# Kernel tuning notes

Hardware: AMD Instinct MI355X
Metric: run time of the kernel (lower is better)

The kernel has to match this reference:

```python
import jax, jax.numpy as jnp
import numpy as np

B1, B2, R, L, D, H = 48, 48, 36, 30, 1024, 4
EPS = 1e-8


def _l2norm(x):
    return x / (jnp.sqrt(jnp.sum(x * x, axis=-1, keepdims=True)) + EPS)


def _summary_attn(x, w1, b1, w2, b2):
    # x: (B1,B2,N,D). MLP scores -> softmax over N -> weighted mean over H heads.
    h = jax.nn.relu(jnp.einsum('abnd,ed->abne', x, w1) + b1)
    s = jnp.einsum('abne,he->abnh', h, w2) + b2          # (B1,B2,N,H)
    p = jax.nn.softmax(jnp.swapaxes(s, -1, -2), axis=-1)  # (B1,B2,H,N)
    w = jnp.einsum('abhn,abnd->abhd', p, x)               # (B1,B2,H,D)
    return w.mean(axis=-2)                                # (B1,B2,D)


def setup_inputs() -> dict:
    key = jax.random.key(0)
    ks = jax.random.split(key, 12)
    r = np.sqrt(6.0) / np.sqrt(D + D)  # xavier uniform as in init_weights
    return {
        'v1': jax.random.normal(ks[0], (B1, R, D), dtype=jnp.float32),
        'v2': jax.random.normal(ks[1], (B2, L, D), dtype=jnp.float32),
        'w_img': jax.random.uniform(ks[2], (D, D), jnp.float32, -r, r),
        'w_txt': jax.random.uniform(ks[3], (D, D), jnp.float32, -r, r),
        'w1a': jax.random.normal(ks[4], (D, D), jnp.float32) * 0.02,
        'b1a': jnp.zeros((D,), jnp.float32),
        'w2a': jax.random.normal(ks[5], (H, D), jnp.float32) * 0.02,
        'b2a': jnp.zeros((H,), jnp.float32),
        'w1b': jax.random.normal(ks[6], (D, D), jnp.float32) * 0.02,
        'b1b': jnp.zeros((D,), jnp.float32),
        'w2b': jax.random.normal(ks[7], (H, D), jnp.float32) * 0.02,
        'b2b': jnp.zeros((H,), jnp.float32),
    }


def reference(v1, v2, w_img, w_txt, w1a, b1a, w2a, b2a, w1b, b1b, w2b, b2b):
    d = v1.shape[-1]
    inv_sqrt_d = np.float32(1.0 / np.sqrt(d))
    k1 = jnp.einsum('ard,ed->are', v1, w_img)  # (B1,R,D)
    k2 = jnp.einsum('bld,ed->ble', v2, w_txt)  # (B2,L,D)

    # qkv_attention(k2, k1, v1): queries=words, keys/values=regions
    s1 = jnp.einsum('bld,ard->ablr', k2, k1) * inv_sqrt_d   # (B1,B2,L,R)
    p1 = jax.nn.softmax(s1, axis=-1)
    fused_v2 = jnp.einsum('ablr,ard->abld', p1, v1)         # weighted_v1 -> fused_v2

    # qkv_attention(k1, k2, v2): queries=regions, keys/values=words
    s2 = jnp.einsum('ard,bld->abrl', k1, k2) * inv_sqrt_d   # (B1,B2,R,L)
    p2 = jax.nn.softmax(s2, axis=-1)
    fused_v1 = jnp.einsum('abrl,bld->abrd', p2, v2)         # weighted_v2 -> fused_v1

    co_v1 = _l2norm(_summary_attn(fused_v1, w1a, b1a, w2a, b2a))
    co_v2 = _l2norm(_summary_attn(fused_v2, w1b, b1b, w2b, b2b))
    return jnp.sum(co_v1 * co_v2, axis=-1)  # (B1,B2) score matrix
```

## Files before the change

kernel.cpp:

```cpp
#include <hip/hip_runtime.h>

#define D 1024
#define NB1 48
#define NB2 48
#define RR 36
#define LL 30
#define NH 4

typedef short bf16x8 __attribute__((ext_vector_type(8)));
typedef float f32x4 __attribute__((ext_vector_type(4)));
typedef float f32x2 __attribute__((ext_vector_type(2)));
typedef unsigned short u16x8 __attribute__((ext_vector_type(8)));

#define MFMA16(a, b, c) __builtin_amdgcn_mfma_f32_16x16x32_bf16(a, b, c, 0, 0, 0)

__device__ __forceinline__ unsigned short f2bf(float x) {
  unsigned u = __float_as_uint(x);
  u += 0x7FFF + ((u >> 16) & 1);
  return (unsigned short)(u >> 16);
}
__device__ __forceinline__ float bf2f(unsigned short h) {
  return __uint_as_float(((unsigned)h) << 16);
}
__device__ __forceinline__ void split8(const float* v, bf16x8& h8, bf16x8& l8) {
  u16x8 hi, lo;
#pragma unroll
  for (int i = 0; i < 8; ++i) {
    unsigned short h = f2bf(v[i]);
    hi[i] = h;
    lo[i] = f2bf(v[i] - bf2f(h));
  }
  h8 = __builtin_bit_cast(bf16x8, hi);
  l8 = __builtin_bit_cast(bf16x8, lo);
}
__device__ __forceinline__ f32x2 shflx2(f32x2 v, int m) {
  double d = __builtin_bit_cast(double, v);
  d = __shfl_xor(d, m);
  return __builtin_bit_cast(f32x2, d);
}

__device__ __forceinline__ void conv_body(const float* __restrict__ X,
                                          unsigned short* __restrict__ out,
                                          int rows, int g) {
  const int lane = threadIdx.x & 63;
  const int tile = g >> 5, kc = g & 31;
  const int row = tile * 16 + (lane & 15);
  const int k = kc * 32 + (lane >> 4) * 8;
  float v[8];
  if (row < rows) {
    const float4* s = (const float4*)(X + (size_t)row * 1024 + k);
    float4 x0 = s[0], x1 = s[1];
    v[0] = x0.x; v[1] = x0.y; v[2] = x0.z; v[3] = x0.w;
    v[4] = x1.x; v[5] = x1.y; v[6] = x1.z; v[7] = x1.w;
  } else {
#pragma unroll
    for (int i = 0; i < 8; ++i) v[i] = 0.f;
  }
  bf16x8 hi, lo;
  split8(v, hi, lo);
  bf16x8* o = (bf16x8*)(out + (size_t)g * 1024 + lane * 8);
  o[0] = hi;
  o[64] = lo;
}

__global__ __launch_bounds__(256) void conv6(
    const float* __restrict__ v1, const float* __restrict__ v2,
    const float* __restrict__ wimg, const float* __restrict__ wtxt,
    const float* __restrict__ w1a, const float* __restrict__ w1b,
    unsigned short* v1f, unsigned short* v2f, unsigned short* wimgf,
    unsigned short* wtxtf, unsigned short* w1af, unsigned short* w1bf) {
  const float* X; unsigned short* O; int rows;
  switch (blockIdx.y) {
    case 0: X = v1; O = v1f; rows = 1728; break;
    case 1: X = v2; O = v2f; rows = 1440; break;
    case 2: X = wimg; O = wimgf; rows = 1024; break;
    case 3: X = wtxt; O = wtxtf; rows = 1024; break;
    case 4: X = w1a; O = w1af; rows = 1024; break;
    default: X = w1b; O = w1bf; rows = 1024; break;
  }
  const int tiles = (rows + 15) >> 4;
  const int g = blockIdx.x * 4 + (threadIdx.x >> 6);
  if (g >= tiles * 32) return;
  conv_body(X, O, rows, g);
}

__global__ __launch_bounds__(256) void conv_k(const float* __restrict__ k1,
                                              const float* __restrict__ k2,
                                              unsigned short* k1f, unsigned short* k2f) {
  const float* X = blockIdx.y ? k2 : k1;
  unsigned short* O = blockIdx.y ? k2f : k1f;
  const int rows = blockIdx.y ? 1440 : 1728;
  const int tiles = (rows + 15) >> 4;
  const int g = blockIdx.x * 4 + (threadIdx.x >> 6);
  if (g >= tiles * 32) return;
  conv_body(X, O, rows, g);
}

__global__ __launch_bounds__(256) void convG(const float* __restrict__ G2a,
                                             const float* __restrict__ G1b,
                                             const float* __restrict__ w2a,
                                             const float* __restrict__ w2b,
                                             unsigned short* G2aF, unsigned short* G1bF,
                                             float4* __restrict__ w2at,
                                             float4* __restrict__ w2bt) {
  const int t = threadIdx.x, lane = t & 63;
  if (blockIdx.y == 0 && blockIdx.x < 4) {
    int col = blockIdx.x * 256 + t;
    w2at[col] = make_float4(w2a[col], w2a[1024 + col], w2a[2048 + col], w2a[3072 + col]);
    w2bt[col] = make_float4(w2b[col], w2b[1024 + col], w2b[2048 + col], w2b[3072 + col]);
  }
  const int bb = blockIdx.x >> 4;
  const int nt = ((blockIdx.x & 15) << 2) + (t >> 6);
  const int c = lane & 15, q = lane >> 4;
  if (blockIdx.y == 0) {
    float v[8];
#pragma unroll
    for (int j = 0; j < 8; ++j) {
      int l = q * 8 + j;
      v[j] = (l < LL) ? G2a[(size_t)(bb * LL + l) * D + nt * 16 + c] : 0.f;
    }
    bf16x8 hi, lo;
    split8(v, hi, lo);
    bf16x8* o = (bf16x8*)(G2aF + ((size_t)(bb * 64 + nt) * 2) * 512 + lane * 8);
    o[0] = hi;
    o[64] = lo;
  } else {
#pragma unroll
    for (int kc = 0; kc < 2; ++kc) {
      float v[8];
#pragma unroll
      for (int j = 0; j < 8; ++j) {
        int r = kc * 32 + q * 8 + j;
        v[j] = (r < RR) ? G1b[(size_t)(bb * RR + r) * D + nt * 16 + c] : 0.f;
      }
      bf16x8 hi, lo;
      split8(v, hi, lo);
      bf16x8* o = (bf16x8*)(G1bF + (((size_t)(bb * 64 + nt) * 2 + kc) * 2) * 512 + lane * 8);
      o[0] = hi;
      o[64] = lo;
    }
  }
}

#define LOAD_FRAGS(AH, AL, BH, BL)                                              \
  {                                                                             \
    _Pragma("unroll") for (int i = 0; i < 4; ++i) {                             \
      AH[i] = Af[ab[i]]; AL[i] = Af[ab[i] + 64]; ab[i] += 128;                  \
    }                                                                           \
    _Pragma("unroll") for (int j = 0; j < 4; ++j) {                             \
      BH[j] = Bf[bb[j]]; BL[j] = Bf[bb[j] + 64]; bb[j] += 128;                  \
    }                                                                           \
  }

#define MFMA_SET(AH, AL, BH, BL)                                                \
  _Pragma("unroll") for (int i = 0; i < 4; ++i)                                 \
      _Pragma("unroll") for (int j = 0; j < 4; ++j) {                           \
    acc[i][j] = MFMA16(AH[i], BH[j], acc[i][j]);                                \
    acc[i][j] = MFMA16(AL[i], BH[j], acc[i][j]);                                \
    acc[i][j] = MFMA16(AH[i], BL[j], acc[i][j]);                                \
  }

__device__ __forceinline__ void gemm4_body(const bf16x8* __restrict__ Af,
                                           const bf16x8* __restrict__ Bf,
                                           float* __restrict__ C,
                                           int M, int N, float scale,
                                           int Mtiles, int Ntiles) {
  const int lane = threadIdx.x & 63;
  const int w = threadIdx.x >> 6;
  const int mb = blockIdx.y * 8 + (w >> 1) * 4;
  const int nb = blockIdx.x * 8 + (w & 1) * 4;
  int ab[4], bb[4];
#pragma unroll
  for (int i = 0; i < 4; ++i) {
    int tm = mb + i; if (tm > Mtiles - 1) tm = Mtiles - 1;
    ab[i] = tm * 4096 + lane;
    int tn = nb + i; if (tn > Ntiles - 1) tn = Ntiles - 1;
    bb[i] = tn * 4096 + lane;
  }
  f32x4 acc[4][4];
#pragma unroll
  for (int i = 0; i < 4; ++i)
#pragma unroll
    for (int j = 0; j < 4; ++j) acc[i][j] = (f32x4){0.f, 0.f, 0.f, 0.f};

  bf16x8 ahA[4], alA[4], bhA[4], blA[4];
  bf16x8 ahB[4], alB[4], bhB[4], blB[4];
  LOAD_FRAGS(ahA, alA, bhA, blA);
#pragma unroll 1
  for (int kc = 0; kc < 30; kc += 2) {
    LOAD_FRAGS(ahB, alB, bhB, blB);
    MFMA_SET(ahA, alA, bhA, blA);
    LOAD_FRAGS(ahA, alA, bhA, blA);
    MFMA_SET(ahB, alB, bhB, blB);
  }
  LOAD_FRAGS(ahB, alB, bhB, blB);
  MFMA_SET(ahA, alA, bhA, blA);
  MFMA_SET(ahB, alB, bhB, blB);

  const int c16 = lane & 15, q = lane >> 4;
#pragma unroll
  for (int i = 0; i < 4; ++i) {
#pragma unroll
    for (int reg = 0; reg < 4; ++reg) {
      int r = (mb + i) * 16 + q * 4 + reg;
      if (r < M) {
#pragma unroll
        for (int j = 0; j < 4; ++j) {
          int col = (nb + j) * 16 + c16;
          if (col < N) C[(size_t)r * N + col] = acc[i][j][reg] * scale;
        }
      }
    }
  }
}

__global__ __launch_bounds__(256) void proj_fused(
    const bf16x8* __restrict__ v1f, const bf16x8* __restrict__ v2f,
    const bf16x8* __restrict__ wimgf, const bf16x8* __restrict__ wtxtf,
    const bf16x8* __restrict__ w1af, const bf16x8* __restrict__ w1bf,
    float* k1, float* k2, float* G2a, float* G1b) {
  const int z = blockIdx.z;
  const bf16x8* Af = (z == 0 || z == 3) ? v1f : v2f;
  const bf16x8* Bf = (z == 0) ? wimgf : (z == 1) ? wtxtf : (z == 2) ? w1af : w1bf;
  float* C = (z == 0) ? k1 : (z == 1) ? k2 : (z == 2) ? G2a : G1b;
  const int M = (z == 0 || z == 3) ? 1728 : 1440;
  const int Mt = (z == 0 || z == 3) ? 108 : 92;
  if ((int)blockIdx.y * 8 >= Mt) return;
  gemm4_body(Af, Bf, C, M, 1024, 1.f, Mt, 64);
}

__global__ __launch_bounds__(256) void cross_s(
    const bf16x8* __restrict__ k2f, const bf16x8* __restrict__ k1f,
    float* Sbuf) {
  gemm4_body(k2f, k1f, Sbuf, 1440, 1728, 0.03125f, 92, 108);
}

__global__ __launch_bounds__(128) void pair_dir(
    const float* __restrict__ Sb,
    const float* __restrict__ v1, const float* __restrict__ v2,
    const bf16x8* __restrict__ G2aF, const bf16x8* __restrict__ G1bF,
    const float* __restrict__ b1a, const float4* __restrict__ w2at, const float* __restrict__ b2a,
    const float* __restrict__ b1b, const float4* __restrict__ w2bt, const float* __restrict__ b2b,
    float* __restrict__ YA, float* __restrict__ YB,
    float* __restrict__ N1buf, float* __restrict__ N2buf) {
  const int pair = blockIdx.x;
  const int a = pair / NB2;
  const int b = pair - a * NB2;
  const int t = threadIdx.x, lane = t & 63, w = t >> 6;
  const int c16 = lane & 15, q = lane >> 4;

  union SM {
    struct {
      float p2s[48][36];
      float red[2][48][4];
      float sa[RR][NH];
      float qa[RR];
      float u2[LL];
      float rb[2];
    } A;
    struct {
      float p1s[32][68];
      float red[2][48][4];
      float sbm[LL][NH];
      float qb[LL];
      float u1[RR];
      float rb[2];
    } B;
  };
  __shared__ __align__(16) SM sm;

  const float* Sab = Sb + (size_t)b * LL * 1728 + (size_t)a * RR;

  if (blockIdx.y == 0) {
    for (int i = t; i < 48 * 36; i += 128) {
      int r = i / 36, c = i - r * 36;
      if (r >= RR || c >= LL) ((float*)sm.A.p2s)[i] = 0.f;
    }
    for (int i = t; i < LL * RR; i += 128) {
      int l = i / RR, r = i - l * RR;
      sm.A.p2s[r][l] = Sab[(size_t)l * 1728 + r];
    }
    __syncthreads();
    if (t < RR * 2) {
      int r = t >> 1, half = t & 1;
      float m = -1e30f;
      for (int l = half; l < LL; l += 2) m = fmaxf(m, sm.A.p2s[r][l]);
      m = fmaxf(m, __shfl_xor(m, 1));
      float s = 0.f;
      for (int l = half; l < LL; l += 2) {
        float e = __expf(sm.A.p2s[r][l] - m);
        sm.A.p2s[r][l] = e;
        s += e;
      }
      s += __shfl_xor(s, 1);
      float inv = 1.f / s;
      for (int l = half; l < LL; l += 2) sm.A.p2s[r][l] *= inv;
    }
    __syncthreads();

    bf16x8 pAh[3], pAl[3];
#pragma unroll
    for (int mt = 0; mt < 3; ++mt) {
      float v[8];
      const float* rp = &sm.A.p2s[mt * 16 + c16][q * 8];
      float4 x0 = *(const float4*)rp;
      float4 x1 = *(const float4*)(rp + 4);
      v[0] = x0.x; v[1] = x0.y; v[2] = x0.z; v[3] = x0.w;
      v[4] = x1.x; v[5] = x1.y; v[6] = x1.z; v[7] = x1.w;
      split8(v, pAh[mt], pAl[mt]);
    }

    f32x2 sc01[3][4], sc23[3][4];
#pragma unroll
    for (int mt = 0; mt < 3; ++mt)
#pragma unroll
      for (int reg = 0; reg < 4; ++reg) {
        sc01[mt][reg] = (f32x2){0.f, 0.f};
        sc23[mt][reg] = (f32x2){0.f, 0.f};
      }

    const bf16x8* gA = G2aF + ((size_t)(b * 64 + w) * 2) * 64 + lane;
#pragma unroll 2
    for (int it = 0; it < 32; ++it) {
      const bf16x8* gp = gA + (size_t)it * 256;
      bf16x8 Bh = gp[0], Bl = gp[64];
      const int col = (w + it * 2) * 16 + c16;
      float4 wv = w2at[col];
      float bias = b1a[col];
      f32x2 w01 = {wv.x, wv.y}, w23 = {wv.z, wv.w};
#pragma unroll
      for (int mt = 0; mt < 3; ++mt) {
        f32x4 acc = {bias, bias, bias, bias};
        acc = MFMA16(pAh[mt], Bh, acc);
        acc = MFMA16(pAl[mt], Bh, acc);
        acc = MFMA16(pAh[mt], Bl, acc);
#pragma unroll
        for (int reg = 0; reg < 4; ++reg) {
          float hv = fmaxf(acc[reg], 0.f);
          f32x2 hv2 = {hv, hv};
          sc01[mt][reg] += hv2 * w01;
          sc23[mt][reg] += hv2 * w23;
        }
      }
    }
#pragma unroll
    for (int mt = 0; mt < 3; ++mt)
#pragma unroll
      for (int reg = 0; reg < 4; ++reg) {
        f32x2 v01 = sc01[mt][reg], v23 = sc23[mt][reg];
#pragma unroll
        for (int m = 1; m <= 8; m <<= 1) {
          v01 += shflx2(v01, m);
          v23 += shflx2(v23, m);
        }
        if (c16 == 0) {
          f32x2* rp = (f32x2*)&sm.A.red[w][mt * 16 + q * 4 + reg][0];
          rp[0] = v01;
          rp[1] = v23;
        }
      }
    __syncthreads();
    for (int i = t; i < RR * NH; i += 128) {
      int r = i >> 2, h = i & 3;
      sm.A.sa[r][h] = sm.A.red[0][r][h] + sm.A.red[1][r][h] + b2a[h];
    }
    __syncthreads();
    if (t < 64) {
      const int h = t >> 4, i = t & 15;
      float x0 = sm.A.sa[i][h];
      float x1 = sm.A.sa[i + 16][h];
      float x2 = (i < 4) ? sm.A.sa[i + 32][h] : -1e30f;
      float m = fmaxf(fmaxf(x0, x1), x2);
      m = fmaxf(m, __shfl_xor(m, 1));
      m = fmaxf(m, __shfl_xor(m, 2));
      m = fmaxf(m, __shfl_xor(m, 4));
      m = fmaxf(m, __shfl_xor(m, 8));
      float e0 = __expf(x0 - m), e1 = __expf(x1 - m);
      float e2 = (i < 4) ? __expf(x2 - m) : 0.f;
      float s = e0 + e1 + e2;
      s += __shfl_xor(s, 1);
      s += __shfl_xor(s, 2);
      s += __shfl_xor(s, 4);
      s += __shfl_xor(s, 8);
      float inv = 1.f / s;
      sm.A.sa[i][h] = e0 * inv;
      sm.A.sa[i + 16][h] = e1 * inv;
      if (i < 4) sm.A.sa[i + 32][h] = e2 * inv;
    }
    __syncthreads();
    if (t < RR)
      sm.A.qa[t] = 0.25f * (sm.A.sa[t][0] + sm.A.sa[t][1] + sm.A.sa[t][2] + sm.A.sa[t][3]);
    __syncthreads();
    if (t < LL * 2) {
      int l = t >> 1, half = t & 1;
      float x = 0.f;
      for (int r = half; r < RR; r += 2) x = fmaf(sm.A.qa[r], sm.A.p2s[r][l], x);
      x += __shfl_xor(x, 1);
      if (half == 0) sm.A.u2[l] = x;
    }
    __syncthreads();
    {
      const float* V2b = v2 + ((size_t)b * LL) * D + t * 8;
      float4 y0 = {0.f, 0.f, 0.f, 0.f}, y1 = {0.f, 0.f, 0.f, 0.f};
      for (int l = 0; l < LL; ++l) {
        float ul = sm.A.u2[l];
        float4 aa = *(const float4*)(V2b + (size_t)l * D);
        float4 cc = *(const float4*)(V2b + (size_t)l * D + 4);
        y0.x = fmaf(ul, aa.x, y0.x); y0.y = fmaf(ul, aa.y, y0.y);
        y0.z = fmaf(ul, aa.z, y0.z); y0.w = fmaf(ul, aa.w, y0.w);
        y1.x = fmaf(ul, cc.x, y1.x); y1.y = fmaf(ul, cc.y, y1.y);
        y1.z = fmaf(ul, cc.z, y1.z); y1.w = fmaf(ul, cc.w, y1.w);
      }
      float4* Yo = (float4*)(YA + (size_t)pair * 1024 + t * 8);
      Yo[0] = y0;
      Yo[1] = y1;
      float pn1 = y0.x * y0.x + y0.y * y0.y + y0.z * y0.z + y0.w * y0.w +
                  y1.x * y1.x + y1.y * y1.y + y1.z * y1.z + y1.w * y1.w;
#pragma unroll
      for (int off = 32; off; off >>= 1) pn1 += __shfl_down(pn1, off);
      if (lane == 0) sm.A.rb[w] = pn1;
      __syncthreads();
      if (t == 0) N1buf[pair] = sm.A.rb[0] + sm.A.rb[1];
    }
  } else {
    for (int i = t; i < 32 * 68; i += 128) {
      int l = i / 68, c = i - l * 68;
      if (l >= LL || c >= RR) ((float*)sm.B.p1s)[i] = 0.f;
    }
    for (int i = t; i < LL * RR; i += 128) {
      int l = i / RR, r = i - l * RR;
      sm.B.p1s[l][r] = Sab[(size_t)l * 1728 + r];
    }
    __syncthreads();
    if (t < LL * 2) {
      int l = t >> 1, half = t & 1;
      float m = -1e30f;
      for (int r = half; r < RR; r += 2) m = fmaxf(m, sm.B.p1s[l][r]);
      m = fmaxf(m, __shfl_xor(m, 1));
      float s = 0.f;
      for (int r = half; r < RR; r += 2) {
        float e = __expf(sm.B.p1s[l][r] - m);
        sm.B.p1s[l][r] = e;
        s += e;
      }
      s += __shfl_xor(s, 1);
      float inv = 1.f / s;
      for (int r = half; r < RR; r += 2) sm.B.p1s[l][r] *= inv;
    }
    __syncthreads();

    bf16x8 pBh[2][2], pBl[2][2];
#pragma unroll
    for (int mt = 0; mt < 2; ++mt)
#pragma unroll
      for (int kc = 0; kc < 2; ++kc) {
        float v[8];
        const float* rp = &sm.B.p1s[mt * 16 + c16][kc * 32 + q * 8];
        float4 x0 = *(const float4*)rp;
        float4 x1 = *(const float4*)(rp + 4);
        v[0] = x0.x; v[1] = x0.y; v[2] = x0.z; v[3] = x0.w;
        v[4] = x1.x; v[5] = x1.y; v[6] = x1.z; v[7] = x1.w;
        split8(v, pBh[mt][kc], pBl[mt][kc]);
      }

    f32x2 sc01[2][4], sc23[2][4];
#pragma unroll
    for (int mt = 0; mt < 2; ++mt)
#pragma unroll
      for (int reg = 0; reg < 4; ++reg) {
        sc01[mt][reg] = (f32x2){0.f, 0.f};
        sc23[mt][reg] = (f32x2){0.f, 0.f};
      }

    const bf16x8* gB = G1bF + ((size_t)(a * 64 + w) * 4) * 64 + lane;
#pragma unroll 2
    for (int it = 0; it < 32; ++it) {
      const bf16x8* gp = gB + (size_t)it * 512;
      bf16x8 B0h = gp[0], B0l = gp[64], B1h = gp[128], B1l = gp[192];
      const int col = (w + it * 2) * 16 + c16;
      float4 wv = w2bt[col];
      float bias = b1b[col];
      f32x2 w01 = {wv.x, wv.y}, w23 = {wv.z, wv.w};
#pragma unroll
      for (int mt = 0; mt < 2; ++mt) {
        f32x4 acc = {bias, bias, bias, bias};
        acc = MFMA16(pBh[mt][0], B0h, acc);
        acc = MFMA16(pBl[mt][0], B0h, acc);
        acc = MFMA16(pBh[mt][0], B0l, acc);
        acc = MFMA16(pBh[mt][1], B1h, acc);
        acc = MFMA16(pBl[mt][1], B1h, acc);
        acc = MFMA16(pBh[mt][1], B1l, acc);
#pragma unroll
        for (int reg = 0; reg < 4; ++reg) {
          float hv = fmaxf(acc[reg], 0.f);
          f32x2 hv2 = {hv, hv};
          sc01[mt][reg] += hv2 * w01;
          sc23[mt][reg] += hv2 * w23;
        }
      }
    }
#pragma unroll
    for (int mt = 0; mt < 2; ++mt)
#pragma unroll
      for (int reg = 0; reg < 4; ++reg) {
        f32x2 v01 = sc01[mt][reg], v23 = sc23[mt][reg];
#pragma unroll
        for (int m = 1; m <= 8; m <<= 1) {
          v01 += shflx2(v01, m);
          v23 += shflx2(v23, m);
        }
        if (c16 == 0) {
          f32x2* rp = (f32x2*)&sm.B.red[w][mt * 16 + q * 4 + reg][0];
          rp[0] = v01;
          rp[1] = v23;
        }
      }
    __syncthreads();
    for (int i = t; i < LL * NH; i += 128) {
      int l = i >> 2, h = i & 3;
      sm.B.sbm[l][h] = sm.B.red[0][l][h] + sm.B.red[1][l][h] + b2b[h];
    }
    __syncthreads();
    if (t < 64) {
      const int h = t >> 4, i = t & 15;
      float x0 = sm.B.sbm[i][h];
      float x1 = (i < 14) ? sm.B.sbm[i + 16][h] : -1e30f;
      float m = fmaxf(x0, x1);
      m = fmaxf(m, __shfl_xor(m, 1));
      m = fmaxf(m, __shfl_xor(m, 2));
      m = fmaxf(m, __shfl_xor(m, 4));
      m = fmaxf(m, __shfl_xor(m, 8));
      float e0 = __expf(x0 - m);
      float e1 = (i < 14) ? __expf(x1 - m) : 0.f;
      float s = e0 + e1;
      s += __shfl_xor(s, 1);
      s += __shfl_xor(s, 2);
      s += __shfl_xor(s, 4);
      s += __shfl_xor(s, 8);
      float inv = 1.f / s;
      sm.B.sbm[i][h] = e0 * inv;
      if (i < 14) sm.B.sbm[i + 16][h] = e1 * inv;
    }
    __syncthreads();
    if (t < LL)
      sm.B.qb[t] = 0.25f * (sm.B.sbm[t][0] + sm.B.sbm[t][1] + sm.B.sbm[t][2] + sm.B.sbm[t][3]);
    __syncthreads();
    if (t < RR * 2) {
      int r = t >> 1, half = t & 1;
      float x = 0.f;
      for (int l = half; l < LL; l += 2) x = fmaf(sm.B.qb[l], sm.B.p1s[l][r], x);
      x += __shfl_xor(x, 1);
      if (half == 0) sm.B.u1[r] = x;
    }
    __syncthreads();
    {
      const float* V1a = v1 + ((size_t)a * RR) * D + t * 8;
      float4 y0 = {0.f, 0.f, 0.f, 0.f}, y1 = {0.f, 0.f, 0.f, 0.f};
      for (int r = 0; r < RR; ++r) {
        float ur = sm.B.u1[r];
        float4 aa = *(const float4*)(V1a + (size_t)r * D);
        float4 cc = *(const float4*)(V1a + (size_t)r * D + 4);
        y0.x = fmaf(ur, aa.x, y0.x); y0.y = fmaf(ur, aa.y, y0.y);
        y0.z = fmaf(ur, aa.z, y0.z); y0.w = fmaf(ur, aa.w, y0.w);
        y1.x = fmaf(ur, cc.x, y1.x); y1.y = fmaf(ur, cc.y, y1.y);
        y1.z = fmaf(ur, cc.z, y1.z); y1.w = fmaf(ur, cc.w, y1.w);
      }
      float4* Yo = (float4*)(YB + (size_t)pair * 1024 + t * 8);
      Yo[0] = y0;
      Yo[1] = y1;
      float pn2 = y0.x * y0.x + y0.y * y0.y + y0.z * y0.z + y0.w * y0.w +
                  y1.x * y1.x + y1.y * y1.y + y1.z * y1.z + y1.w * y1.w;
#pragma unroll
      for (int off = 32; off; off >>= 1) pn2 += __shfl_down(pn2, off);
      if (lane == 0) sm.B.rb[w] = pn2;
      __syncthreads();
      if (t == 0) N2buf[pair] = sm.B.rb[0] + sm.B.rb[1];
    }
  }
}

__global__ __launch_bounds__(128) void pair_final(
    const float* __restrict__ YA, const float* __restrict__ YB,
    const float* __restrict__ N1buf, const float* __restrict__ N2buf,
    float* __restrict__ out) {
  const int pair = blockIdx.x;
  const int t = threadIdx.x;
  const float4* ya = (const float4*)(YA + (size_t)pair * 1024);
  const float4* yb = (const float4*)(YB + (size_t)pair * 1024);
  float s = 0.f;
#pragma unroll
  for (int i = 0; i < 2; ++i) {
    float4 a = ya[t + i * 128], b = yb[t + i * 128];
    s += a.x * b.x + a.y * b.y + a.z * b.z + a.w * b.w;
  }
#pragma unroll
  for (int off = 32; off; off >>= 1) s += __shfl_down(s, off);
  __shared__ float r2[2];
  if ((t & 63) == 0) r2[t >> 6] = s;
  __syncthreads();
  if (t == 0) {
    float num = r2[0] + r2[1];
    float n1 = sqrtf(fmaxf(N1buf[pair], 0.f));
    float n2 = sqrtf(fmaxf(N2buf[pair], 0.f));
    out[pair] = num / ((n1 + 1e-8f) * (n2 + 1e-8f));
  }
}

extern "C" void kernel_launch(void* const* d_in, const int* in_sizes, int n_in,
                              void* d_out, int out_size, void* d_ws, size_t ws_size,
                              hipStream_t stream) {
  const float* v1    = (const float*)d_in[0];
  const float* v2    = (const float*)d_in[1];
  const float* w_img = (const float*)d_in[2];
  const float* w_txt = (const float*)d_in[3];
  const float* w1a   = (const float*)d_in[4];
  const float* b1a   = (const float*)d_in[5];
  const float* w2a   = (const float*)d_in[6];
  const float* b2a   = (const float*)d_in[7];
  const float* w1b   = (const float*)d_in[8];
  const float* b1b   = (const float*)d_in[9];
  const float* w2b   = (const float*)d_in[10];
  const float* b2b   = (const float*)d_in[11];
  float* out = (float*)d_out;

  float* ws   = (float*)d_ws;
  float* k1   = ws;
  float* k2   = k1 + (size_t)1728 * 1024;
  float* G2a  = k2 + (size_t)1440 * 1024;
  float* G1b  = G2a + (size_t)1440 * 1024;
  float* Sbuf = G1b + (size_t)1728 * 1024;
  float* Cbuf = Sbuf + (size_t)1440 * 1728;
  float* g22  = Cbuf + (size_t)1440 * 1728;
  float* g11  = g22 + (size_t)48 * 900;
  (void)g22; (void)g11;

  unsigned short* fb    = (unsigned short*)(g11 + (size_t)48 * 1296);
  unsigned short* v1f   = fb;
  unsigned short* v2f   = v1f + (size_t)108 * 32768;
  unsigned short* k1f   = v2f + (size_t)92 * 32768;
  unsigned short* k2f   = k1f + (size_t)108 * 32768;
  unsigned short* wimgf = k2f + (size_t)92 * 32768;
  unsigned short* wtxtf = wimgf + (size_t)64 * 32768;
  unsigned short* w1af  = wtxtf + (size_t)64 * 32768;
  unsigned short* w1bf  = w1af + (size_t)64 * 32768;
  unsigned short* G2aF  = w1bf + (size_t)64 * 32768;
  unsigned short* G1bF  = G2aF + (size_t)48 * 65536;

  float4* w2at = (float4*)k1;
  float4* w2bt = w2at + 1024;

  float* YA = Cbuf;
  float* YB = (float*)k1f;
  float* N1buf = G2a;
  float* N2buf = N1buf + 2304;

  conv6<<<dim3(864, 6), 256, 0, stream>>>(v1, v2, w_img, w_txt, w1a, w1b,
                                          v1f, v2f, wimgf, wtxtf, w1af, w1bf);

  proj_fused<<<dim3(8, 14, 4), 256, 0, stream>>>(
      (const bf16x8*)v1f, (const bf16x8*)v2f, (const bf16x8*)wimgf,
      (const bf16x8*)wtxtf, (const bf16x8*)w1af, (const bf16x8*)w1bf,
      k1, k2, G2a, G1b);

  conv_k<<<dim3(864, 2), 256, 0, stream>>>(k1, k2, k1f, k2f);
  convG<<<dim3(768, 2), 256, 0, stream>>>(G2a, G1b, w2a, w2b, G2aF, G1bF, w2at, w2bt);

  cross_s<<<dim3(14, 12), 256, 0, stream>>>(
      (const bf16x8*)k2f, (const bf16x8*)k1f, Sbuf);

  pair_dir<<<dim3(2304, 2), 128, 0, stream>>>(
      Sbuf, v1, v2, (const bf16x8*)G2aF, (const bf16x8*)G1bF,
      b1a, w2at, b2a, b1b, w2bt, b2b, YA, YB, N1buf, N2buf);
  pair_final<<<2304, 128, 0, stream>>>(YA, YB, N1buf, N2buf, out);
}
```

Measured before the change: 313.2 us.

## Give each wavefront one pair-direction and batch the value projection per block

pair_dir now gives each 64-lane wave a whole (pair, direction) task. Per-wave shared memory and sched barriers replace the block-wide __syncthreads, and each wave loops over all 64 column tiles itself. The final weighted sum over v1/v2 moves into a new y_batch kernel that reuses each loaded v row across all 48 partners held in registers. pair_final now computes the norms itself. The aim is to cut sync overhead and repeated global reads of v. In exchange it adds a kernel launch, MFMA setprio hints and more register pressure from the 48-entry accumulators.

```diff
diff --git a/kernel.cpp b/kernel.cpp
--- a/kernel.cpp
+++ b/kernel.cpp
@@ -235,74 +235,56 @@
   gemm4_body(k2f, k1f, Sbuf, 1440, 1728, 0.03125f, 92, 108);
 }
 
-__global__ __launch_bounds__(128) void pair_dir(
+__global__ __launch_bounds__(256, 4) void pair_dir(
     const float* __restrict__ Sb,
-    const float* __restrict__ v1, const float* __restrict__ v2,
     const bf16x8* __restrict__ G2aF, const bf16x8* __restrict__ G1bF,
     const float* __restrict__ b1a, const float4* __restrict__ w2at, const float* __restrict__ b2a,
     const float* __restrict__ b1b, const float4* __restrict__ w2bt, const float* __restrict__ b2b,
-    float* __restrict__ YA, float* __restrict__ YB,
-    float* __restrict__ N1buf, float* __restrict__ N2buf) {
-  const int pair = blockIdx.x;
+    float* __restrict__ U1buf, float* __restrict__ U2buf) {
+  const int t = threadIdx.x, lane = t & 63, w = t >> 6;
+  const int id = blockIdx.x * 4 + w;
+  const int pair = id >> 1, dir = id & 1;
   const int a = pair / NB2;
   const int b = pair - a * NB2;
-  const int t = threadIdx.x, lane = t & 63, w = t >> 6;
   const int c16 = lane & 15, q = lane >> 4;
 
-  union SM {
-    struct {
-      float p2s[48][36];
-      float red[2][48][4];
-      float sa[RR][NH];
-      float qa[RR];
-      float u2[LL];
-      float rb[2];
-    } A;
-    struct {
-      float p1s[32][68];
-      float red[2][48][4];
-      float sbm[LL][NH];
-      float qb[LL];
-      float u1[RR];
-      float rb[2];
-    } B;
+  union WSM {
+    struct { float p2s[48][36]; float sa[48][NH]; float qa[48]; } A;
+    struct { float p1s[32][68]; float sbm[32][NH]; float qb[32]; } B;
   };
-  __shared__ __align__(16) SM sm;
-
-  const float* Sab = Sb + (size_t)b * LL * 1728 + (size_t)a * RR;
-
-  if (blockIdx.y == 0) {
-    for (int i = t; i < 48 * 36; i += 128) {
-      int r = i / 36, c = i - r * 36;
-      if (r >= RR || c >= LL) ((float*)sm.A.p2s)[i] = 0.f;
-    }
-    for (int i = t; i < LL * RR; i += 128) {
+  __shared__ __align__(16) WSM sm[4];
+  WSM& S = sm[w];
+
+  const float* Sab = Sb + (size_t)(b * LL) * 1728 + a * RR;
+
+  if (dir == 0) {
+    for (int i = lane; i < 48 * 36; i += 64) ((float*)S.A.p2s)[i] = 0.f;
+    __builtin_amdgcn_sched_barrier(0);
+    for (int i = lane; i < LL * RR; i += 64) {
       int l = i / RR, r = i - l * RR;
-      sm.A.p2s[r][l] = Sab[(size_t)l * 1728 + r];
-    }
-    __syncthreads();
-    if (t < RR * 2) {
-      int r = t >> 1, half = t & 1;
+      S.A.p2s[r][l] = Sab[(size_t)l * 1728 + r];
+    }
+    __builtin_amdgcn_sched_barrier(0);
+    if (lane < RR) {
+      const int r = lane;
       float m = -1e30f;
-      for (int l = half; l < LL; l += 2) m = fmaxf(m, sm.A.p2s[r][l]);
-      m = fmaxf(m, __shfl_xor(m, 1));
+      for (int l = 0; l < LL; ++l) m = fmaxf(m, S.A.p2s[r][l]);
       float s = 0.f;
-      for (int l = half; l < LL; l += 2) {
-        float e = __expf(sm.A.p2s[r][l] - m);
-        sm.A.p2s[r][l] = e;
+      for (int l = 0; l < LL; ++l) {
+        float e = __expf(S.A.p2s[r][l] - m);
+        S.A.p2s[r][l] = e;
         s += e;
       }
-      s += __shfl_xor(s, 1);
       float inv = 1.f / s;
-      for (int l = half; l < LL; l += 2) sm.A.p2s[r][l] *= inv;
-    }
-    __syncthreads();
+      for (int l = 0; l < LL; ++l) S.A.p2s[r][l] *= inv;
+    }
+    __builtin_amdgcn_sched_barrier(0);
 
     bf16x8 pAh[3], pAl[3];
 #pragma unroll
     for (int mt = 0; mt < 3; ++mt) {
       float v[8];
-      const float* rp = &sm.A.p2s[mt * 16 + c16][q * 8];
+      const float* rp = &S.A.p2s[mt * 16 + c16][q * 8];
       float4 x0 = *(const float4*)rp;
       float4 x1 = *(const float4*)(rp + 4);
       v[0] = x0.x; v[1] = x0.y; v[2] = x0.z; v[3] = x0.w;
@@ -319,21 +301,23 @@
         sc23[mt][reg] = (f32x2){0.f, 0.f};
       }
 
-    const bf16x8* gA = G2aF + ((size_t)(b * 64 + w) * 2) * 64 + lane;
+    const bf16x8* gA = G2aF + (size_t)(b * 64) * 128 + lane;
 #pragma unroll 2
-    for (int it = 0; it < 32; ++it) {
-      const bf16x8* gp = gA + (size_t)it * 256;
+    for (int it = 0; it < 64; ++it) {
+      const bf16x8* gp = gA + (size_t)it * 128;
       bf16x8 Bh = gp[0], Bl = gp[64];
-      const int col = (w + it * 2) * 16 + c16;
+      const int col = it * 16 + c16;
       float4 wv = w2at[col];
       float bias = b1a[col];
       f32x2 w01 = {wv.x, wv.y}, w23 = {wv.z, wv.w};
 #pragma unroll
       for (int mt = 0; mt < 3; ++mt) {
         f32x4 acc = {bias, bias, bias, bias};
+        __builtin_amdgcn_s_setprio(1);
         acc = MFMA16(pAh[mt], Bh, acc);
         acc = MFMA16(pAl[mt], Bh, acc);
         acc = MFMA16(pAh[mt], Bl, acc);
+        __builtin_amdgcn_s_setprio(0);
 #pragma unroll
         for (int reg = 0; reg < 4; ++reg) {
           float hv = fmaxf(acc[reg], 0.f);
@@ -343,6 +327,7 @@
         }
       }
     }
+    f32x2 b01 = {b2a[0], b2a[1]}, b23 = {b2a[2], b2a[3]};
 #pragma unroll
     for (int mt = 0; mt < 3; ++mt)
 #pragma unroll
@@ -354,22 +339,17 @@
           v23 += shflx2(v23, m);
         }
         if (c16 == 0) {
-          f32x2* rp = (f32x2*)&sm.A.red[w][mt * 16 + q * 4 + reg][0];
-          rp[0] = v01;
-          rp[1] = v23;
+          f32x2* rp = (f32x2*)&S.A.sa[mt * 16 + q * 4 + reg][0];
+          rp[0] = v01 + b01;
+          rp[1] = v23 + b23;
         }
       }
-    __syncthreads();
-    for (int i = t; i < RR * NH; i += 128) {
-      int r = i >> 2, h = i & 3;
-      sm.A.sa[r][h] = sm.A.red[0][r][h] + sm.A.red[1][r][h] + b2a[h];
-    }
-    __syncthreads();
-    if (t < 64) {
-      const int h = t >> 4, i = t & 15;
-      float x0 = sm.A.sa[i][h];
-      float x1 = sm.A.sa[i + 16][h];
-      float x2 = (i < 4) ? sm.A.sa[i + 32][h] : -1e30f;
+    __builtin_amdgcn_sched_barrier(0);
+    {
+      const int h = q, i = c16;
+      float x0 = S.A.sa[i][h];
+      float x1 = S.A.sa[i + 16][h];
+      float x2 = (i < 4) ? S.A.sa[i + 32][h] : -1e30f;
       float m = fmaxf(fmaxf(x0, x1), x2);
       m = fmaxf(m, __shfl_xor(m, 1));
       m = fmaxf(m, __shfl_xor(m, 2));
@@ -382,72 +362,46 @@
       s += __shfl_xor(s, 2);
       s += __shfl_xor(s, 4);
       s += __shfl_xor(s, 8);
+      float inv = 0.25f / s;
+      float p0 = e0 * inv, p1 = e1 * inv, p2v = e2 * inv;
+      p0 += __shfl_xor(p0, 16); p0 += __shfl_xor(p0, 32);
+      p1 += __shfl_xor(p1, 16); p1 += __shfl_xor(p1, 32);
+      p2v += __shfl_xor(p2v, 16); p2v += __shfl_xor(p2v, 32);
+      if (q == 0) {
+        S.A.qa[i] = p0;
+        S.A.qa[i + 16] = p1;
+        if (i < 4) S.A.qa[i + 32] = p2v;
+      }
+    }
+    __builtin_amdgcn_sched_barrier(0);
+    if (lane < LL) {
+      const int l = lane;
+      float x = 0.f;
+      for (int r = 0; r < RR; ++r) x = fmaf(S.A.qa[r], S.A.p2s[r][l], x);
+      U2buf[((size_t)b * 48 + a) * 32 + l] = x;
+    }
+  } else {
+    for (int i = lane; i < 32 * 68; i += 64) ((float*)S.B.p1s)[i] = 0.f;
+    __builtin_amdgcn_sched_barrier(0);
+    for (int i = lane; i < LL * RR; i += 64) {
+      int l = i / RR, r = i - l * RR;
+      S.B.p1s[l][r] = Sab[(size_t)l * 1728 + r];
+    }
+    __builtin_amdgcn_sched_barrier(0);
+    if (lane < LL) {
+      const int l = lane;
+      float m = -1e30f;
+      for (int r = 0; r < RR; ++r) m = fmaxf(m, S.B.p1s[l][r]);
+      float s = 0.f;
+      for (int r = 0; r < RR; ++r) {
+        float e = __expf(S.B.p1s[l][r] - m);
+        S.B.p1s[l][r] = e;
+        s += e;
+      }
       float inv = 1.f / s;
-      sm.A.sa[i][h] = e0 * inv;
-      sm.A.sa[i + 16][h] = e1 * inv;
-      if (i < 4) sm.A.sa[i + 32][h] = e2 * inv;
-    }
-    __syncthreads();
-    if (t < RR)
-      sm.A.qa[t] = 0.25f * (sm.A.sa[t][0] + sm.A.sa[t][1] + sm.A.sa[t][2] + sm.A.sa[t][3]);
-    __syncthreads();
-    if (t < LL * 2) {
-      int l = t >> 1, half = t & 1;
-      float x = 0.f;
-      for (int r = half; r < RR; r += 2) x = fmaf(sm.A.qa[r], sm.A.p2s[r][l], x);
-      x += __shfl_xor(x, 1);
-      if (half == 0) sm.A.u2[l] = x;
-    }
-    __syncthreads();
-    {
-      const float* V2b = v2 + ((size_t)b * LL) * D + t * 8;
-      float4 y0 = {0.f, 0.f, 0.f, 0.f}, y1 = {0.f, 0.f, 0.f, 0.f};
-      for (int l = 0; l < LL; ++l) {
-        float ul = sm.A.u2[l];
-        float4 aa = *(const float4*)(V2b + (size_t)l * D);
-        float4 cc = *(const float4*)(V2b + (size_t)l * D + 4);
-        y0.x = fmaf(ul, aa.x, y0.x); y0.y = fmaf(ul, aa.y, y0.y);
-        y0.z = fmaf(ul, aa.z, y0.z); y0.w = fmaf(ul, aa.w, y0.w);
-        y1.x = fmaf(ul, cc.x, y1.x); y1.y = fmaf(ul, cc.y, y1.y);
-        y1.z = fmaf(ul, cc.z, y1.z); y1.w = fmaf(ul, cc.w, y1.w);
-      }
-      float4* Yo = (float4*)(YA + (size_t)pair * 1024 + t * 8);
-      Yo[0] = y0;
-      Yo[1] = y1;
-      float pn1 = y0.x * y0.x + y0.y * y0.y + y0.z * y0.z + y0.w * y0.w +
-                  y1.x * y1.x + y1.y * y1.y + y1.z * y1.z + y1.w * y1.w;
-#pragma unroll
-      for (int off = 32; off; off >>= 1) pn1 += __shfl_down(pn1, off);
-      if (lane == 0) sm.A.rb[w] = pn1;
-      __syncthreads();
-      if (t == 0) N1buf[pair] = sm.A.rb[0] + sm.A.rb[1];
-    }
-  } else {
-    for (int i = t; i < 32 * 68; i += 128) {
-      int l = i / 68, c = i - l * 68;
-      if (l >= LL || c >= RR) ((float*)sm.B.p1s)[i] = 0.f;
-    }
-    for (int i = t; i < LL * RR; i += 128) {
-      int l = i / RR, r = i - l * RR;
-      sm.B.p1s[l][r] = Sab[(size_t)l * 1728 + r];
-    }
-    __syncthreads();
-    if (t < LL * 2) {
-      int l = t >> 1, half = t & 1;
-      float m = -1e30f;
-      for (int r = half; r < RR; r += 2) m = fmaxf(m, sm.B.p1s[l][r]);
-      m = fmaxf(m, __shfl_xor(m, 1));
-      float s = 0.f;
-      for (int r = half; r < RR; r += 2) {
-        float e = __expf(sm.B.p1s[l][r] - m);
-        sm.B.p1s[l][r] = e;
-        s += e;
-      }
-      s += __shfl_xor(s, 1);
-      float inv = 1.f / s;
-      for (int r = half; r < RR; r += 2) sm.B.p1s[l][r] *= inv;
-    }
-    __syncthreads();
+      for (int r = 0; r < RR; ++r) S.B.p1s[l][r] *= inv;
+    }
+    __builtin_amdgcn_sched_barrier(0);
 
     bf16x8 pBh[2][2], pBl[2][2];
 #pragma unroll
@@ -455,7 +409,7 @@
 #pragma unroll
       for (int kc = 0; kc < 2; ++kc) {
         float v[8];
-        const float* rp = &sm.B.p1s[mt * 16 + c16][kc * 32 + q * 8];
+        const float* rp = &S.B.p1s[mt * 16 + c16][kc * 32 + q * 8];
         float4 x0 = *(const float4*)rp;
         float4 x1 = *(const float4*)(rp + 4);
         v[0] = x0.x; v[1] = x0.y; v[2] = x0.z; v[3] = x0.w;
@@ -472,24 +426,26 @@
         sc23[mt][reg] = (f32x2){0.f, 0.f};
       }
 
-    const bf16x8* gB = G1bF + ((size_t)(a * 64 + w) * 4) * 64 + lane;
+    const bf16x8* gB = G1bF + (size_t)(a * 64) * 256 + lane;
 #pragma unroll 2
-    for (int it = 0; it < 32; ++it) {
-      const bf16x8* gp = gB + (size_t)it * 512;
+    for (int it = 0; it < 64; ++it) {
+      const bf16x8* gp = gB + (size_t)it * 256;
       bf16x8 B0h = gp[0], B0l = gp[64], B1h = gp[128], B1l = gp[192];
-      const int col = (w + it * 2) * 16 + c16;
+      const int col = it * 16 + c16;
       float4 wv = w2bt[col];
       float bias = b1b[col];
       f32x2 w01 = {wv.x, wv.y}, w23 = {wv.z, wv.w};
 #pragma unroll
       for (int mt = 0; mt < 2; ++mt) {
         f32x4 acc = {bias, bias, bias, bias};
+        __builtin_amdgcn_s_setprio(1);
         acc = MFMA16(pBh[mt][0], B0h, acc);
         acc = MFMA16(pBl[mt][0], B0h, acc);
         acc = MFMA16(pBh[mt][0], B0l, acc);
         acc = MFMA16(pBh[mt][1], B1h, acc);
         acc = MFMA16(pBl[mt][1], B1h, acc);
         acc = MFMA16(pBh[mt][1], B1l, acc);
+        __builtin_amdgcn_s_setprio(0);
 #pragma unroll
         for (int reg = 0; reg < 4; ++reg) {
           float hv = fmaxf(acc[reg], 0.f);
@@ -499,6 +455,7 @@
         }
       }
     }
+    f32x2 b01 = {b2b[0], b2b[1]}, b23 = {b2b[2], b2b[3]};
 #pragma unroll
     for (int mt = 0; mt < 2; ++mt)
 #pragma unroll
@@ -510,21 +467,16 @@
           v23 += shflx2(v23, m);
         }
         if (c16 == 0) {
-          f32x2* rp = (f32x2*)&sm.B.red[w][mt * 16 + q * 4 + reg][0];
-          rp[0] = v01;
-          rp[1] = v23;
+          f32x2* rp = (f32x2*)&S.B.sbm[mt * 16 + q * 4 + reg][0];
+          rp[0] = v01 + b01;
+          rp[1] = v23 + b23;
         }
       }
-    __syncthreads();
-    for (int i = t; i < LL * NH; i += 128) {
-      int l = i >> 2, h = i & 3;
-      sm.B.sbm[l][h] = sm.B.red[0][l][h] + sm.B.red[1][l][h] + b2b[h];
-    }
-    __syncthreads();
-    if (t < 64) {
-      const int h = t >> 4, i = t & 15;
-      float x0 = sm.B.sbm[i][h];
-      float x1 = (i < 14) ? sm.B.sbm[i + 16][h] : -1e30f;
+    __builtin_amdgcn_sched_barrier(0);
+    {
+      const int h = q, i = c16;
+      float x0 = S.B.sbm[i][h];
+      float x1 = (i < 14) ? S.B.sbm[i + 16][h] : -1e30f;
       float m = fmaxf(x0, x1);
       m = fmaxf(m, __shfl_xor(m, 1));
       m = fmaxf(m, __shfl_xor(m, 2));
@@ -537,72 +489,91 @@
       s += __shfl_xor(s, 2);
       s += __shfl_xor(s, 4);
       s += __shfl_xor(s, 8);
-      float inv = 1.f / s;
-      sm.B.sbm[i][h] = e0 * inv;
-      if (i < 14) sm.B.sbm[i + 16][h] = e1 * inv;
-    }
+      float inv = 0.25f / s;
+      float p0 = e0 * inv, p1 = e1 * inv;
+      p0 += __shfl_xor(p0, 16); p0 += __shfl_xor(p0, 32);
+      p1 += __shfl_xor(p1, 16); p1 += __shfl_xor(p1, 32);
+      if (q == 0) {
+        S.B.qb[i] = p0;
+        if (i < 14) S.B.qb[i + 16] = p1;
+      }
+    }
+    __builtin_amdgcn_sched_barrier(0);
+    if (lane < RR) {
+      const int r = lane;
+      float x = 0.f;
+      for (int l = 0; l < LL; ++l) x = fmaf(S.B.qb[l], S.B.p1s[l][r], x);
+      U1buf[((size_t)a * 48 + b) * 40 + r] = x;
+    }
+  }
+}
+
+__global__ __launch_bounds__(256) void y_batch(
+    const float* __restrict__ v1, const float* __restrict__ v2,
+    const float* __restrict__ U1buf, const float* __restrict__ U2buf,
+    float* __restrict__ YA, float* __restrict__ YB) {
+  const int bb = blockIdx.x;
+  const int col = blockIdx.z * 256 + threadIdx.x;
+  __shared__ float us[48 * 40];
+  float y[48];
+#pragma unroll
+  for (int i = 0; i < 48; ++i) y[i] = 0.f;
+  if (blockIdx.y == 0) {
+    for (int i = threadIdx.x; i < 48 * 32; i += 256) us[i] = U2buf[(size_t)bb * 1536 + i];
     __syncthreads();
-    if (t < LL)
-      sm.B.qb[t] = 0.25f * (sm.B.sbm[t][0] + sm.B.sbm[t][1] + sm.B.sbm[t][2] + sm.B.sbm[t][3]);
+    const float* V = v2 + (size_t)bb * LL * 1024 + col;
+    for (int l = 0; l < LL; ++l) {
+      float v = V[(size_t)l * 1024];
+#pragma unroll
+      for (int i = 0; i < 48; ++i) y[i] = fmaf(us[i * 32 + l], v, y[i]);
+    }
+    float* Yo = YA + (size_t)bb * 48 * 1024 + col;
+#pragma unroll
+    for (int i = 0; i < 48; ++i) Yo[(size_t)i * 1024] = y[i];
+  } else {
+    for (int i = threadIdx.x; i < 48 * 40; i += 256) us[i] = U1buf[(size_t)bb * 1920 + i];
     __syncthreads();
-    if (t < RR * 2) {
-      int r = t >> 1, half = t & 1;
-      float x = 0.f;
-      for (int l = half; l < LL; l += 2) x = fmaf(sm.B.qb[l], sm.B.p1s[l][r], x);
-      x += __shfl_xor(x, 1);
-      if (half == 0) sm.B.u1[r] = x;
-    }
-    __syncthreads();
-    {
-      const float* V1a = v1 + ((size_t)a * RR) * D + t * 8;
-      float4 y0 = {0.f, 0.f, 0.f, 0.f}, y1 = {0.f, 0.f, 0.f, 0.f};
-      for (int r = 0; r < RR; ++r) {
-        float ur = sm.B.u1[r];
-        float4 aa = *(const float4*)(V1a + (size_t)r * D);
-        float4 cc = *(const float4*)(V1a + (size_t)r * D + 4);
-        y0.x = fmaf(ur, aa.x, y0.x); y0.y = fmaf(ur, aa.y, y0.y);
-        y0.z = fmaf(ur, aa.z, y0.z); y0.w = fmaf(ur, aa.w, y0.w);
-        y1.x = fmaf(ur, cc.x, y1.x); y1.y = fmaf(ur, cc.y, y1.y);
-        y1.z = fmaf(ur, cc.z, y1.z); y1.w = fmaf(ur, cc.w, y1.w);
-      }
-      float4* Yo = (float4*)(YB + (size_t)pair * 1024 + t * 8);
-      Yo[0] = y0;
-      Yo[1] = y1;
-      float pn2 = y0.x * y0.x + y0.y * y0.y + y0.z * y0.z + y0.w * y0.w +
-                  y1.x * y1.x + y1.y * y1.y + y1.z * y1.z + y1.w * y1.w;
-#pragma unroll
-      for (int off = 32; off; off >>= 1) pn2 += __shfl_down(pn2, off);
-      if (lane == 0) sm.B.rb[w] = pn2;
-      __syncthreads();
-      if (t == 0) N2buf[pair] = sm.B.rb[0] + sm.B.rb[1];
-    }
-  }
-}
-
-__global__ __launch_bounds__(128) void pair_final(
+    const float* V = v1 + (size_t)bb * RR * 1024 + col;
+    for (int r = 0; r < RR; ++r) {
+      float v = V[(size_t)r * 1024];
+#pragma unroll
+      for (int i = 0; i < 48; ++i) y[i] = fmaf(us[i * 40 + r], v, y[i]);
+    }
+    float* Yo = YB + (size_t)bb * 48 * 1024 + col;
+#pragma unroll
+    for (int i = 0; i < 48; ++i) Yo[(size_t)i * 1024] = y[i];
+  }
+}
+
+__global__ __launch_bounds__(256) void pair_final(
     const float* __restrict__ YA, const float* __restrict__ YB,
-    const float* __restrict__ N1buf, const float* __restrict__ N2buf,
     float* __restrict__ out) {
   const int pair = blockIdx.x;
+  const int a = pair / NB2;
+  const int b = pair - a * NB2;
   const int t = threadIdx.x;
-  const float4* ya = (const float4*)(YA + (size_t)pair * 1024);
-  const float4* yb = (const float4*)(YB + (size_t)pair * 1024);
-  float s = 0.f;
-#pragma unroll
-  for (int i = 0; i < 2; ++i) {
-    float4 a = ya[t + i * 128], b = yb[t + i * 128];
-    s += a.x * b.x + a.y * b.y + a.z * b.z + a.w * b.w;
-  }
-#pragma unroll
-  for (int off = 32; off; off >>= 1) s += __shfl_down(s, off);
-  __shared__ float r2[2];
-  if ((t & 63) == 0) r2[t >> 6] = s;
+  const float4* ya = (const float4*)(YA + ((size_t)b * 48 + a) * 1024);
+  const float4* yb = (const float4*)(YB + ((size_t)a * 48 + b) * 1024);
+  float4 va = ya[t], vb = yb[t];
+  float num = va.x * vb.x + va.y * vb.y + va.z * vb.z + va.w * vb.w;
+  float n1 = va.x * va.x + va.y * va.y + va.z * va.z + va.w * va.w;
+  float n2 = vb.x * vb.x + vb.y * vb.y + vb.z * vb.z + vb.w * vb.w;
+#pragma unroll
+  for (int off = 32; off; off >>= 1) {
+    num += __shfl_down(num, off);
+    n1 += __shfl_down(n1, off);
+    n2 += __shfl_down(n2, off);
+  }
+  __shared__ float r3[3][4];
+  if ((t & 63) == 0) {
+    r3[0][t >> 6] = num; r3[1][t >> 6] = n1; r3[2][t >> 6] = n2;
+  }
   __syncthreads();
   if (t == 0) {
-    float num = r2[0] + r2[1];
-    float n1 = sqrtf(fmaxf(N1buf[pair], 0.f));
-    float n2 = sqrtf(fmaxf(N2buf[pair], 0.f));
-    out[pair] = num / ((n1 + 1e-8f) * (n2 + 1e-8f));
+    float nu = r3[0][0] + r3[0][1] + r3[0][2] + r3[0][3];
+    float s1 = sqrtf(fmaxf(r3[1][0] + r3[1][1] + r3[1][2] + r3[1][3], 0.f));
+    float s2 = sqrtf(fmaxf(r3[2][0] + r3[2][1] + r3[2][2] + r3[2][3], 0.f));
+    out[pair] = nu / ((s1 + 1e-8f) * (s2 + 1e-8f));
   }
 }
 
@@ -632,7 +603,6 @@
   float* Cbuf = Sbuf + (size_t)1440 * 1728;
   float* g22  = Cbuf + (size_t)1440 * 1728;
   float* g11  = g22 + (size_t)48 * 900;
-  (void)g22; (void)g11;
 
   unsigned short* fb    = (unsigned short*)(g11 + (size_t)48 * 1296);
   unsigned short* v1f   = fb;
@@ -649,10 +619,10 @@
   float4* w2at = (float4*)k1;
   float4* w2bt = w2at + 1024;
 
+  float* U2buf = G2a;
+  float* U1buf = U2buf + (size_t)48 * 48 * 32;
   float* YA = Cbuf;
   float* YB = (float*)k1f;
-  float* N1buf = G2a;
-  float* N2buf = N1buf + 2304;
 
   conv6<<<dim3(864, 6), 256, 0, stream>>>(v1, v2, w_img, w_txt, w1a, w1b,
                                           v1f, v2f, wimgf, wtxtf, w1af, w1bf);
@@ -668,8 +638,9 @@
   cross_s<<<dim3(14, 12), 256, 0, stream>>>(
       (const bf16x8*)k2f, (const bf16x8*)k1f, Sbuf);
 
-  pair_dir<<<dim3(2304, 2), 128, 0, stream>>>(
-      Sbuf, v1, v2, (const bf16x8*)G2aF, (const bf16x8*)G1bF,
-      b1a, w2at, b2a, b1b, w2bt, b2b, YA, YB, N1buf, N2buf);
-  pair_final<<<2304, 128, 0, stream>>>(YA, YB, N1buf, N2buf, out);
-}
+  pair_dir<<<1152, 256, 0, stream>>>(
+      Sbuf, (const bf16x8*)G2aF, (const bf16x8*)G1bF,
+      b1a, w2at, b2a, b1b, w2bt, b2b, U1buf, U2buf);
+  y_batch<<<dim3(48, 2, 4), 256, 0, stream>>>(v1, v2, U1buf, U2buf, YA, YB);
+  pair_final<<<2304, 256, 0, stream>>>(YA, YB, out);
+}
```

New measurement: 295.6 us. -5.6%, faster.
